# Kernel tuning notes

Measured on AMD Instinct MI355X. Metric: run time of the kernel, lower is better.

## Reference

```python
import jax, jax.numpy as jnp
import numpy as np

DIM = 1024
HID = 4096
E = 8
K = 3


def setup_inputs() -> dict:
    key = jax.random.key(0)
    ks = jax.random.split(key, 5)
    x = jax.random.normal(ks[0], (2, 2048, DIM), dtype=jnp.float32)
    # router: nn.Linear(dim, E) -- initialized to zero in source, but we use small
    # random weights so routing is non-degenerate for the correctness baseline.
    router_w = jax.random.normal(ks[1], (E, DIM), dtype=jnp.float32) * 0.02
    router_b = jax.random.normal(ks[2], (E,), dtype=jnp.float32) * 0.02
    # per-expert SwiGLU params: w12: [E, dim, 2*hid], w3: [E, hid, dim]
    w12 = jax.random.normal(ks[3], (E, DIM, 2 * HID), dtype=jnp.float32) * 0.02
    w3 = jax.random.normal(ks[4], (E, HID, DIM), dtype=jnp.float32) * 0.02
    return {"x": x, "router_w": router_w, "router_b": router_b, "w12": w12, "w3": w3}


def _moe(x, router_w, router_b, w12, w3):
    # router logits [B, S, E]
    logits = jnp.einsum("bsd,ed->bse", x, router_w) + router_b
    scores = jax.nn.sigmoid(logits)
    topk_scores, topk_idx = jax.lax.top_k(scores, K)  # [B,S,K]
    weights = topk_scores / (topk_scores.sum(axis=-1, keepdims=True) + 1e-6)
    # dense per-expert combine weight [B, S, E] (zero if expert not selected)
    onehot = jax.nn.one_hot(topk_idx, E, dtype=x.dtype)  # [B,S,K,E]
    dense_w = jnp.einsum("bske,bsk->bse", onehot, weights)
    out = jnp.zeros_like(x)
    for e in range(E):  # small fixed structural loop over experts
        x12 = x @ w12[e]  # [B,S,2H]
        x1, x2 = jnp.split(x12, 2, axis=-1)
        hidden = jax.nn.silu(x1) * x2
        out = out + (hidden @ w3[e]) * dense_w[..., e:e + 1]
    aux_loss = 0.01 * jnp.mean(logits ** 2)
    return out, aux_loss


def reference(x, router_w, router_b, w12, w3):
    return _moe(x, router_w, router_b, w12, w3)
```

## Files before the change

kernel.cpp:

```cpp
#include <hip/hip_runtime.h>
#include <math.h>

typedef unsigned short u16;
typedef __bf16 bf16x8 __attribute__((ext_vector_type(8)));
typedef float f32x4 __attribute__((ext_vector_type(4)));

#define T_TOK 4096
#define DIM   1024
#define HID   4096
#define NE    8
#define TOPK  3
#define NPAIR 12288

#define PREP_W3_BASE  1024
#define PREP_W12_BASE 3072
#define PREP_BLOCKS   7168

constexpr size_t OFF_CTRL = 0;
constexpr size_t OFF_XB   = 256;
constexpr size_t OFF_W12T = OFF_XB   + (size_t)T_TOK * DIM * 2;
constexpr size_t OFF_W3T  = OFF_W12T + (size_t)NE * 2 * HID * DIM * 2;
constexpr size_t OFF_HID  = OFF_W3T  + (size_t)NE * DIM * HID * 2;
constexpr size_t OFF_Y    = OFF_HID  + (size_t)NPAIR * HID * 2;
constexpr size_t OFF_PTOK = OFF_Y    + (size_t)NPAIR * DIM * 4;
constexpr size_t OFF_TE   = OFF_PTOK + (size_t)NPAIR * 4;
constexpr size_t OFF_TW   = OFF_TE   + (size_t)T_TOK * TOPK * 4;
constexpr size_t OFF_TS   = OFF_TW   + (size_t)T_TOK * TOPK * 4;

__device__ __forceinline__ u16 f2bf(float f) {
    unsigned u = __builtin_bit_cast(unsigned, f);
    u += 0x7fffu + ((u >> 16) & 1u);
    return (u16)(u >> 16);
}

__device__ __forceinline__ void ld_g2l(const u16* g, u16* l) {
    __builtin_amdgcn_global_load_lds((__attribute__((address_space(1))) unsigned*)(g),
                                     (__attribute__((address_space(3))) unsigned*)(l),
                                     16, 0, 0);
}

#define VMCNT(N) asm volatile("s_waitcnt vmcnt(" #N ")" ::: "memory")
#define LGKM0  asm volatile("s_waitcnt lgkmcnt(0)" ::: "memory")
#define SBAR   __builtin_amdgcn_s_barrier()
#define SCHED0 __builtin_amdgcn_sched_barrier(0)
#define PRIO1  __builtin_amdgcn_s_setprio(1)
#define PRIO0  __builtin_amdgcn_s_setprio(0)

#define STAGE_A02(dst) { ld_g2l(srcA[0], (dst) + (0 * 64 + wave * 8) * 64); \
                         ld_g2l(srcA[2], (dst) + (2 * 64 + wave * 8) * 64); }
#define STAGE_B01(dst) { ld_g2l(srcB[0], (dst) + 16384 + (0 * 64 + wave * 8) * 64); \
                         ld_g2l(srcB[1], (dst) + 16384 + (1 * 64 + wave * 8) * 64); }
#define STAGE_B23(dst) { ld_g2l(srcB[2], (dst) + 16384 + (2 * 64 + wave * 8) * 64); \
                         ld_g2l(srcB[3], (dst) + 16384 + (3 * 64 + wave * 8) * 64); }
#define STAGE_A13(dst) { ld_g2l(srcA[1], (dst) + (1 * 64 + wave * 8) * 64); \
                         ld_g2l(srcA[3], (dst) + (3 * 64 + wave * 8) * 64); }
#define ADV()          { _Pragma("unroll") \
                         for (int r_ = 0; r_ < 4; ++r_) { srcA[r_] += 64; srcB[r_] += 64; } }

__device__ __forceinline__ void tc_tile(const float* __restrict__ inp,
                                        u16* __restrict__ outp,
                                        int K, int N, int n0, int k0, int tid,
                                        u16 (*lt)[72]) {
    const int k = tid >> 2;
    const int cbase = (tid & 3) * 4;
    const float* row = inp + (size_t)(k0 + k) * N + n0;
#pragma unroll
    for (int j = 0; j < 16; ++j) {
        const int c = cbase + j * 16;
        float4 f = *(const float4*)(row + c);
        lt[c + 0][k] = f2bf(f.x);
        lt[c + 1][k] = f2bf(f.y);
        lt[c + 2][k] = f2bf(f.z);
        lt[c + 3][k] = f2bf(f.w);
    }
    __syncthreads();
    const int rg = tid >> 2;
    const int kc = (tid & 3) * 16;
#pragma unroll
    for (int g = 0; g < 4; ++g) {
        const int n = g * 64 + rg;
        u16* op = outp + (size_t)(n0 + n) * K + k0 + kc;
        *(uint4*)(op)     = *(const uint4*)(&lt[n][kc]);
        *(uint4*)(op + 8) = *(const uint4*)(&lt[n][kc + 8]);
    }
}

__global__ __launch_bounds__(256) void prep_kernel(const float* __restrict__ x,
                                                   const float* __restrict__ rw,
                                                   const float* __restrict__ rb,
                                                   u16* __restrict__ xb,
                                                   int* __restrict__ tok_expert,
                                                   float* __restrict__ tok_w,
                                                   int* __restrict__ ctrl,
                                                   float* __restrict__ aux,
                                                   const float* __restrict__ w12,
                                                   u16* __restrict__ w12t,
                                                   const float* __restrict__ w3,
                                                   u16* __restrict__ w3t) {
    __shared__ __align__(16) u16 lt[256][72];
    const int bid = blockIdx.x;
    const int tid = threadIdx.x;

    if (bid >= PREP_W12_BASE) {
        const int b = bid - PREP_W12_BASE;
        const int z = b >> 9;
        const int r = b & 511;
        const int kt = r >> 5, nt = r & 31;
        tc_tile(w12 + (size_t)z * DIM * 2 * HID, w12t + (size_t)z * DIM * 2 * HID,
                DIM, 2 * HID, nt * 256, kt * 64, tid, lt);
        return;
    }
    if (bid >= PREP_W3_BASE) {
        const int b = bid - PREP_W3_BASE;
        const int z = b >> 8;
        const int r = b & 255;
        const int kt = r >> 2, nt = r & 3;
        tc_tile(w3 + (size_t)z * HID * DIM, w3t + (size_t)z * HID * DIM,
                HID, DIM, nt * 256, kt * 64, tid, lt);
        return;
    }

    int* hist = (int*)&lt[0][0];
    float* auxsh = (float*)&lt[2][0];
    if (tid < NE) hist[tid] = 0;
    if (tid == NE) auxsh[0] = 0.f;
    __syncthreads();

    const int wave = tid >> 6, lane = tid & 63;
    const int t = bid * 4 + wave;
    const float* xr = x + (size_t)t * DIM;
    u16* xbr = xb + (size_t)t * DIM;

    float p[NE];
#pragma unroll
    for (int e = 0; e < NE; e++) p[e] = 0.f;
#pragma unroll
    for (int q = 0; q < 4; ++q) {
        const int d = q * 256 + lane * 4;
        float4 f = *(const float4*)(xr + d);
        uint2 v;
        v.x = (unsigned)f2bf(f.x) | ((unsigned)f2bf(f.y) << 16);
        v.y = (unsigned)f2bf(f.z) | ((unsigned)f2bf(f.w) << 16);
        *(uint2*)(xbr + d) = v;
#pragma unroll
        for (int e = 0; e < NE; e++) {
            float4 w = *(const float4*)(rw + e * DIM + d);
            p[e] += f.x * w.x + f.y * w.y + f.z * w.z + f.w * w.w;
        }
    }
#pragma unroll
    for (int e = 0; e < NE; e++) {
#pragma unroll
        for (int off = 32; off; off >>= 1) p[e] += __shfl_down(p[e], off, 64);
    }
    if (lane == 0) {
        float s[NE]; float auxs = 0.f;
#pragma unroll
        for (int e = 0; e < NE; e++) {
            float lg = p[e] + rb[e];
            auxs += lg * lg;
            s[e] = 1.f / (1.f + __expf(-lg));
        }
        atomicAdd(auxsh, auxs);
        unsigned mask = 0; float wsum = 0.f;
        int idxs[TOPK]; float vals[TOPK];
        for (int k = 0; k < TOPK; k++) {
            float best = -1.f; int bi = 0;
            for (int e = 0; e < NE; e++)
                if (!((mask >> e) & 1u) && s[e] > best) { best = s[e]; bi = e; }
            mask |= 1u << bi; idxs[k] = bi; vals[k] = best; wsum += best;
        }
        wsum += 1e-6f;
        for (int k = 0; k < TOPK; k++) {
            tok_expert[t * TOPK + k] = idxs[k];
            tok_w[t * TOPK + k] = vals[k] / wsum;
            atomicAdd(&hist[idxs[k]], 1);
        }
    }
    __syncthreads();
    if (tid < NE) { int h = hist[tid]; if (h) atomicAdd(&ctrl[tid], h); }
    if (tid == NE) atomicAdd(aux, auxsh[0] * (0.01f / 32768.0f));
}

__global__ __launch_bounds__(256) void assign_kernel(const int* __restrict__ tok_expert,
                                                     int* __restrict__ ctrl,
                                                     int* __restrict__ pair_token,
                                                     int* __restrict__ tok_slot) {
    __shared__ int soff[NE];
    __shared__ int hist[NE];
    __shared__ int base[NE];
    const int tid = threadIdx.x;
    if (tid < NE) {
        int acc = 0;
        for (int i = 0; i < tid; ++i) acc += ctrl[i];
        soff[tid] = acc;
        hist[tid] = 0;
    }
    __syncthreads();
    const int t = blockIdx.x * blockDim.x + tid;
    int e[TOPK], p[TOPK];
#pragma unroll
    for (int k = 0; k < TOPK; k++) {
        e[k] = tok_expert[t * TOPK + k];
        p[k] = atomicAdd(&hist[e[k]], 1);
    }
    __syncthreads();
    if (tid < NE && hist[tid]) base[tid] = atomicAdd(&ctrl[16 + tid], hist[tid]);
    __syncthreads();
#pragma unroll
    for (int k = 0; k < TOPK; k++) {
        const int slot = soff[e[k]] + base[e[k]] + p[k];
        pair_token[slot] = t;
        tok_slot[t * TOPK + k] = slot;
    }
}

__global__ __launch_bounds__(512, 2) void gemm1_kernel(const u16* __restrict__ xb,
                                                       const u16* __restrict__ w12t,
                                                       const int* __restrict__ pair_token,
                                                       const int* __restrict__ ctrl,
                                                       u16* __restrict__ hidden) {
    const int e = blockIdx.z;
    const int cnt = ctrl[e];
    if ((int)blockIdx.y * 256 >= cnt) return;
    int off = 0;
    for (int i = 0; i < e; ++i) off += ctrl[i];
    const int rowbase = off + blockIdx.y * 256;
    const int rowend = off + cnt;
    const int n0 = blockIdx.x * 128;

    extern __shared__ __align__(16) u16 lds[];

    const int tid = threadIdx.x;
    const int wave = tid >> 6, lane = tid & 63;
    const int srow = tid >> 3;
    const int scol = ((tid & 7) ^ (srow & 7)) * 8;

    const u16* srcA[4];
    const u16* srcB[4];
#pragma unroll
    for (int r = 0; r < 4; ++r) {
        int sr = rowbase + r * 64 + srow;
        int tok = (sr < rowend) ? pair_token[sr] : 0;
        srcA[r] = xb + (size_t)tok * DIM + scol;
    }
#pragma unroll
    for (int r = 0; r < 2; ++r) {
        srcB[r]     = w12t + ((size_t)e * 2 * HID + n0 + r * 64 + srow) * DIM + scol;
        srcB[r + 2] = srcB[r] + (size_t)HID * DIM;
    }

    const int wm = wave >> 2, wn = wave & 3;
    const int lrow = lane & 15, lq = lane >> 4, xm = lrow & 7;
    const int so0 = ((lq ^ xm) << 3);
    const int so1 = (((4 | lq) ^ xm) << 3);

    f32x4 acc0[8][2], acc1[8][2];
#pragma unroll
    for (int mf = 0; mf < 8; ++mf)
#pragma unroll
        for (int nf = 0; nf < 2; ++nf) { acc0[mf][nf] = (f32x4)0.f; acc1[mf][nf] = (f32x4)0.f; }

    STAGE_A02(lds); STAGE_B01(lds);
    STAGE_B23(lds);
    STAGE_A13(lds);
    ADV();

    const int NT = DIM / 64;
    for (int kt = 0; kt < NT; ++kt) {
        u16* cur = lds + (kt & 1) * 32768;
        u16* nxt = lds + ((kt & 1) ^ 1) * 32768;
        const u16* sA = cur;
        const u16* sB = cur + 16384;
        const bool notlast = (kt < NT - 1);

        bf16x8 a[4][2], b0[2][2], b1[2][2];
        VMCNT(4); SBAR; SCHED0;
#pragma unroll
        for (int mf = 0; mf < 4; ++mf) {
            const u16* base = sA + (wm * 128 + mf * 16 + lrow) * 64;
            a[mf][0] = *(const bf16x8*)(base + so0);
            a[mf][1] = *(const bf16x8*)(base + so1);
        }
#pragma unroll
        for (int nf = 0; nf < 2; ++nf) {
            const u16* base = sB + (wn * 32 + nf * 16 + lrow) * 64;
            b0[nf][0] = *(const bf16x8*)(base + so0);
            b0[nf][1] = *(const bf16x8*)(base + so1);
        }
        if (notlast) { STAGE_A02(nxt); STAGE_B01(nxt); }
        LGKM0; SCHED0;
        PRIO1;
#pragma unroll
        for (int mf = 0; mf < 4; ++mf)
#pragma unroll
            for (int nf = 0; nf < 2; ++nf) {
                acc0[mf][nf] = __builtin_amdgcn_mfma_f32_16x16x32_bf16(a[mf][0], b0[nf][0], acc0[mf][nf], 0, 0, 0);
                acc0[mf][nf] = __builtin_amdgcn_mfma_f32_16x16x32_bf16(a[mf][1], b0[nf][1], acc0[mf][nf], 0, 0, 0);
            }
        PRIO0;
        if (notlast) { VMCNT(6); } else { VMCNT(2); }
        SBAR; SCHED0;
#pragma unroll
        for (int nf = 0; nf < 2; ++nf) {
            const u16* base = sB + 128 * 64 + (wn * 32 + nf * 16 + lrow) * 64;
            b1[nf][0] = *(const bf16x8*)(base + so0);
            b1[nf][1] = *(const bf16x8*)(base + so1);
        }
        if (notlast) STAGE_B23(nxt);
        LGKM0; SCHED0;
        PRIO1;
#pragma unroll
        for (int mf = 0; mf < 4; ++mf)
#pragma unroll
            for (int nf = 0; nf < 2; ++nf) {
                acc1[mf][nf] = __builtin_amdgcn_mfma_f32_16x16x32_bf16(a[mf][0], b1[nf][0], acc1[mf][nf], 0, 0, 0);
                acc1[mf][nf] = __builtin_amdgcn_mfma_f32_16x16x32_bf16(a[mf][1], b1[nf][1], acc1[mf][nf], 0, 0, 0);
            }
        PRIO0;
        if (notlast) { VMCNT(6); } else { VMCNT(0); }
        SBAR; SCHED0;
#pragma unroll
        for (int mf = 0; mf < 4; ++mf) {
            const u16* base = sA + (wm * 128 + (mf + 4) * 16 + lrow) * 64;
            a[mf][0] = *(const bf16x8*)(base + so0);
            a[mf][1] = *(const bf16x8*)(base + so1);
        }
        if (notlast) { STAGE_A13(nxt); ADV(); }
        LGKM0; SCHED0;
        PRIO1;
#pragma unroll
        for (int mf = 0; mf < 4; ++mf)
#pragma unroll
            for (int nf = 0; nf < 2; ++nf) {
                acc1[mf + 4][nf] = __builtin_amdgcn_mfma_f32_16x16x32_bf16(a[mf][0], b1[nf][0], acc1[mf + 4][nf], 0, 0, 0);
                acc1[mf + 4][nf] = __builtin_amdgcn_mfma_f32_16x16x32_bf16(a[mf][1], b1[nf][1], acc1[mf + 4][nf], 0, 0, 0);
            }
        PRIO0;
        SBAR;
        PRIO1;
#pragma unroll
        for (int mf = 0; mf < 4; ++mf)
#pragma unroll
            for (int nf = 0; nf < 2; ++nf) {
                acc0[mf + 4][nf] = __builtin_amdgcn_mfma_f32_16x16x32_bf16(a[mf][0], b0[nf][0], acc0[mf + 4][nf], 0, 0, 0);
                acc0[mf + 4][nf] = __builtin_amdgcn_mfma_f32_16x16x32_bf16(a[mf][1], b0[nf][1], acc0[mf + 4][nf], 0, 0, 0);
            }
        PRIO0;
    }

#pragma unroll
    for (int mf = 0; mf < 8; ++mf) {
        const int gr0 = rowbase + wm * 128 + mf * 16 + lq * 4;
#pragma unroll
        for (int nf = 0; nf < 2; ++nf) {
            const int gc = n0 + wn * 32 + nf * 16 + lrow;
#pragma unroll
            for (int r = 0; r < 4; ++r) {
                const int gr = gr0 + r;
                if (gr < rowend) {
                    float x1 = acc0[mf][nf][r], x2 = acc1[mf][nf][r];
                    float h = x1 / (1.f + __expf(-x1)) * x2;
                    hidden[(size_t)gr * HID + gc] = f2bf(h);
                }
            }
        }
    }
}

__global__ __launch_bounds__(512, 2) void gemm2_kernel(const u16* __restrict__ hidden,
                                                       const u16* __restrict__ w3t,
                                                       const int* __restrict__ ctrl,
                                                       float* __restrict__ ybuf) {
    const int e = blockIdx.z;
    const int cnt = ctrl[e];
    if ((int)blockIdx.y * 256 >= cnt) return;
    int off = 0;
    for (int i = 0; i < e; ++i) off += ctrl[i];
    const int rowbase = off + blockIdx.y * 256;
    const int rowend = off + cnt;
    const int n0 = blockIdx.x * 256;

    extern __shared__ __align__(16) u16 lds[];

    const int tid = threadIdx.x;
    const int wave = tid >> 6, lane = tid & 63;
    const int srow = tid >> 3;
    const int scol = ((tid & 7) ^ (srow & 7)) * 8;

    const u16* srcA[4];
    const u16* srcB[4];
#pragma unroll
    for (int r = 0; r < 4; ++r) {
        int sr = rowbase + r * 64 + srow;
        if (sr > NPAIR - 1) sr = NPAIR - 1;
        srcA[r] = hidden + (size_t)sr * HID + scol;
        srcB[r] = w3t + ((size_t)e * DIM + n0 + r * 64 + srow) * HID + scol;
    }

    const int wm = wave >> 2, wn = wave & 3;
    const int lrow = lane & 15, lq = lane >> 4, xm = lrow & 7;
    const int so0 = ((lq ^ xm) << 3);
    const int so1 = (((4 | lq) ^ xm) << 3);

    f32x4 acc[8][4];
#pragma unroll
    for (int mf = 0; mf < 8; ++mf)
#pragma unroll
        for (int nf = 0; nf < 4; ++nf) acc[mf][nf] = (f32x4)0.f;

    STAGE_A02(lds); STAGE_B01(lds);
    STAGE_B23(lds);
    STAGE_A13(lds);
    ADV();

    const int NT = HID / 64;
    for (int kt = 0; kt < NT; ++kt) {
        u16* cur = lds + (kt & 1) * 32768;
        u16* nxt = lds + ((kt & 1) ^ 1) * 32768;
        const u16* sA = cur;
        const u16* sB = cur + 16384;
        const bool notlast = (kt < NT - 1);

        bf16x8 a[4][2], b[4][2];
        VMCNT(4); SBAR; SCHED0;
#pragma unroll
        for (int mf = 0; mf < 4; ++mf) {
            const u16* base = sA + (wm * 128 + mf * 16 + lrow) * 64;
            a[mf][0] = *(const bf16x8*)(base + so0);
            a[mf][1] = *(const bf16x8*)(base + so1);
        }
#pragma unroll
        for (int nf = 0; nf < 2; ++nf) {
            const u16* base = sB + (nf * 64 + wn * 16 + lrow) * 64;
            b[nf][0] = *(const bf16x8*)(base + so0);
            b[nf][1] = *(const bf16x8*)(base + so1);
        }
        if (notlast) { STAGE_A02(nxt); STAGE_B01(nxt); }
        LGKM0; SCHED0;
        PRIO1;
#pragma unroll
        for (int mf = 0; mf < 4; ++mf)
#pragma unroll
            for (int nf = 0; nf < 2; ++nf) {
                acc[mf][nf] = __builtin_amdgcn_mfma_f32_16x16x32_bf16(a[mf][0], b[nf][0], acc[mf][nf], 0, 0, 0);
                acc[mf][nf] = __builtin_amdgcn_mfma_f32_16x16x32_bf16(a[mf][1], b[nf][1], acc[mf][nf], 0, 0, 0);
            }
        PRIO0;
        if (notlast) { VMCNT(6); } else { VMCNT(2); }
        SBAR; SCHED0;
#pragma unroll
        for (int nf = 2; nf < 4; ++nf) {
            const u16* base = sB + (nf * 64 + wn * 16 + lrow) * 64;
            b[nf][0] = *(const bf16x8*)(base + so0);
            b[nf][1] = *(const bf16x8*)(base + so1);
        }
        if (notlast) STAGE_B23(nxt);
        LGKM0; SCHED0;
        PRIO1;
#pragma unroll
        for (int mf = 0; mf < 4; ++mf)
#pragma unroll
            for (int nf = 2; nf < 4; ++nf) {
                acc[mf][nf] = __builtin_amdgcn_mfma_f32_16x16x32_bf16(a[mf][0], b[nf][0], acc[mf][nf], 0, 0, 0);
                acc[mf][nf] = __builtin_amdgcn_mfma_f32_16x16x32_bf16(a[mf][1], b[nf][1], acc[mf][nf], 0, 0, 0);
            }
        PRIO0;
        if (notlast) { VMCNT(6); } else { VMCNT(0); }
        SBAR; SCHED0;
#pragma unroll
        for (int mf = 0; mf < 4; ++mf) {
            const u16* base = sA + (wm * 128 + (mf + 4) * 16 + lrow) * 64;
            a[mf][0] = *(const bf16x8*)(base + so0);
            a[mf][1] = *(const bf16x8*)(base + so1);
        }
        if (notlast) { STAGE_A13(nxt); ADV(); }
        LGKM0; SCHED0;
        PRIO1;
#pragma unroll
        for (int mf = 0; mf < 4; ++mf)
#pragma unroll
            for (int nf = 2; nf < 4; ++nf) {
                acc[mf + 4][nf] = __builtin_amdgcn_mfma_f32_16x16x32_bf16(a[mf][0], b[nf][0], acc[mf + 4][nf], 0, 0, 0);
                acc[mf + 4][nf] = __builtin_amdgcn_mfma_f32_16x16x32_bf16(a[mf][1], b[nf][1], acc[mf + 4][nf], 0, 0, 0);
            }
        PRIO0;
        SBAR;
        PRIO1;
#pragma unroll
        for (int mf = 0; mf < 4; ++mf)
#pragma unroll
            for (int nf = 0; nf < 2; ++nf) {
                acc[mf + 4][nf] = __builtin_amdgcn_mfma_f32_16x16x32_bf16(a[mf][0], b[nf][0], acc[mf + 4][nf], 0, 0, 0);
                acc[mf + 4][nf] = __builtin_amdgcn_mfma_f32_16x16x32_bf16(a[mf][1], b[nf][1], acc[mf + 4][nf], 0, 0, 0);
            }
        PRIO0;
    }

#pragma unroll
    for (int mf = 0; mf < 8; ++mf) {
        const int gr0 = rowbase + wm * 128 + mf * 16 + lq * 4;
#pragma unroll
        for (int nf = 0; nf < 4; ++nf) {
            const int gc = n0 + nf * 64 + wn * 16 + lrow;
#pragma unroll
            for (int r = 0; r < 4; ++r) {
                const int gr = gr0 + r;
                if (gr < rowend) ybuf[(size_t)gr * DIM + gc] = acc[mf][nf][r];
            }
        }
    }
}

__global__ __launch_bounds__(256) void combine_kernel(const float* __restrict__ ybuf,
                                                      const int* __restrict__ tok_slot,
                                                      const float* __restrict__ tok_w,
                                                      float* __restrict__ out) {
    const int t = blockIdx.x;
    const int d = threadIdx.x * 4;
    const int s0 = tok_slot[t * 3 + 0], s1 = tok_slot[t * 3 + 1], s2 = tok_slot[t * 3 + 2];
    const float w0 = tok_w[t * 3 + 0], w1 = tok_w[t * 3 + 1], w2 = tok_w[t * 3 + 2];
    const float4 a0 = *(const float4*)(ybuf + (size_t)s0 * DIM + d);
    const float4 a1 = *(const float4*)(ybuf + (size_t)s1 * DIM + d);
    const float4 a2 = *(const float4*)(ybuf + (size_t)s2 * DIM + d);
    float4 o;
    o.x = w0 * a0.x + w1 * a1.x + w2 * a2.x;
    o.y = w0 * a0.y + w1 * a1.y + w2 * a2.y;
    o.z = w0 * a0.z + w1 * a1.z + w2 * a2.z;
    o.w = w0 * a0.w + w1 * a1.w + w2 * a2.w;
    *(float4*)(out + (size_t)t * DIM + d) = o;
}

extern "C" void kernel_launch(void* const* d_in, const int* in_sizes, int n_in,
                              void* d_out, int out_size, void* d_ws, size_t ws_size,
                              hipStream_t stream) {
    const float* x   = (const float*)d_in[0];
    const float* rw  = (const float*)d_in[1];
    const float* rb  = (const float*)d_in[2];
    const float* w12 = (const float*)d_in[3];
    const float* w3  = (const float*)d_in[4];
    float* out = (float*)d_out;
    char* ws = (char*)d_ws;

    int*   ctrl       = (int*)(ws + OFF_CTRL);
    u16*   xb         = (u16*)(ws + OFF_XB);
    u16*   w12t       = (u16*)(ws + OFF_W12T);
    u16*   w3t        = (u16*)(ws + OFF_W3T);
    u16*   hidden     = (u16*)(ws + OFF_HID);
    float* ybuf       = (float*)(ws + OFF_Y);
    int*   pair_token = (int*)(ws + OFF_PTOK);
    int*   tok_expert = (int*)(ws + OFF_TE);
    float* tok_w      = (float*)(ws + OFF_TW);
    int*   tok_slot   = (int*)(ws + OFF_TS);

    static bool attr_set = false;
    if (!attr_set) {
        hipFuncSetAttribute((const void*)gemm1_kernel, hipFuncAttributeMaxDynamicSharedMemorySize, 131072);
        hipFuncSetAttribute((const void*)gemm2_kernel, hipFuncAttributeMaxDynamicSharedMemorySize, 131072);
        attr_set = true;
    }

    hipMemsetAsync(ctrl, 0, 256, stream);
    hipMemsetAsync(out + (size_t)T_TOK * DIM, 0, sizeof(float), stream);

    prep_kernel<<<PREP_BLOCKS, 256, 0, stream>>>(x, rw, rb, xb, tok_expert, tok_w, ctrl,
                                                 out + (size_t)T_TOK * DIM, w12, w12t, w3, w3t);
    assign_kernel<<<16, 256, 0, stream>>>(tok_expert, ctrl, pair_token, tok_slot);

    gemm1_kernel<<<dim3(HID / 128, 16, NE), 512, 131072, stream>>>(xb, w12t, pair_token, ctrl, hidden);
    gemm2_kernel<<<dim3(DIM / 256, 16, NE), 512, 131072, stream>>>(hidden, w3t, ctrl, ybuf);
    combine_kernel<<<T_TOK, 256, 0, stream>>>(ybuf, tok_slot, tok_w, out);
    (void)in_sizes; (void)n_in; (void)out_size; (void)ws_size;
}
```

Measured before the change: 805.4 us.

## Move w3 weight transpose into gemm1 launch and persist w12 transpose blocks

The w3 fp32-to-bf16 transpose leaves the prep kernel and runs as an extra z-slice of the gemm1 grid, so it overlaps with the expert GEMM1 work. The w12 transpose now uses 256 blocks that each loop over 16 k-tiles, replacing 4096 one-shot blocks and cutting the prep grid. This removes serialized weight-conversion time before gemm1 and reduces block launch overhead. The risk is that the transpose blocks compete with GEMM blocks for CUs and LDS, and the fewer w12 blocks may leave the prep phase with less parallelism.

```diff
diff --git a/kernel.cpp b/kernel.cpp
--- a/kernel.cpp
+++ b/kernel.cpp
@@ -12,9 +12,8 @@
 #define TOPK  3
 #define NPAIR 12288
 
-#define PREP_W3_BASE  1024
-#define PREP_W12_BASE 3072
-#define PREP_BLOCKS   7168
+#define PREP_RTR_BASE 256
+#define PREP_BLOCKS   1280
 
 constexpr size_t OFF_CTRL = 0;
 constexpr size_t OFF_XB   = 256;
@@ -57,10 +56,10 @@
 #define ADV()          { _Pragma("unroll") \
                          for (int r_ = 0; r_ < 4; ++r_) { srcA[r_] += 64; srcB[r_] += 64; } }
 
-__device__ __forceinline__ void tc_tile(const float* __restrict__ inp,
-                                        u16* __restrict__ outp,
-                                        int K, int N, int n0, int k0, int tid,
-                                        u16 (*lt)[72]) {
+__device__ __forceinline__ void tc_tile256(const float* __restrict__ inp,
+                                           u16* __restrict__ outp,
+                                           int K, int N, int n0, int k0, int tid,
+                                           u16 (*lt)[72]) {
     const int k = tid >> 2;
     const int cbase = (tid & 3) * 4;
     const float* row = inp + (size_t)(k0 + k) * N + n0;
@@ -94,29 +93,20 @@
                                                    int* __restrict__ ctrl,
                                                    float* __restrict__ aux,
                                                    const float* __restrict__ w12,
-                                                   u16* __restrict__ w12t,
-                                                   const float* __restrict__ w3,
-                                                   u16* __restrict__ w3t) {
+                                                   u16* __restrict__ w12t) {
     __shared__ __align__(16) u16 lt[256][72];
     const int bid = blockIdx.x;
     const int tid = threadIdx.x;
 
-    if (bid >= PREP_W12_BASE) {
-        const int b = bid - PREP_W12_BASE;
-        const int z = b >> 9;
-        const int r = b & 511;
-        const int kt = r >> 5, nt = r & 31;
-        tc_tile(w12 + (size_t)z * DIM * 2 * HID, w12t + (size_t)z * DIM * 2 * HID,
-                DIM, 2 * HID, nt * 256, kt * 64, tid, lt);
-        return;
-    }
-    if (bid >= PREP_W3_BASE) {
-        const int b = bid - PREP_W3_BASE;
-        const int z = b >> 8;
-        const int r = b & 255;
-        const int kt = r >> 2, nt = r & 3;
-        tc_tile(w3 + (size_t)z * HID * DIM, w3t + (size_t)z * HID * DIM,
-                HID, DIM, nt * 256, kt * 64, tid, lt);
+    if (bid < PREP_RTR_BASE) {
+        const int z = bid >> 5;
+        const int nt = bid & 31;
+        const float* src = w12 + (size_t)z * DIM * 2 * HID;
+        u16* dst = w12t + (size_t)z * DIM * 2 * HID;
+        for (int kt = 0; kt < 16; ++kt) {
+            tc_tile256(src, dst, DIM, 2 * HID, nt * 256, kt * 64, tid, lt);
+            __syncthreads();
+        }
         return;
     }
 
@@ -127,7 +117,7 @@
     __syncthreads();
 
     const int wave = tid >> 6, lane = tid & 63;
-    const int t = bid * 4 + wave;
+    const int t = (bid - PREP_RTR_BASE) * 4 + wave;
     const float* xr = x + (size_t)t * DIM;
     u16* xbr = xb + (size_t)t * DIM;
 
@@ -219,7 +209,49 @@
                                                        const u16* __restrict__ w12t,
                                                        const int* __restrict__ pair_token,
                                                        const int* __restrict__ ctrl,
-                                                       u16* __restrict__ hidden) {
+                                                       u16* __restrict__ hidden,
+                                                       const float* __restrict__ w3,
+                                                       u16* __restrict__ w3t) {
+    extern __shared__ __align__(16) u16 lds[];
+    const int tid = threadIdx.x;
+
+    if (blockIdx.z == 8) {
+        u16 (*lt)[72] = (u16(*)[72])lds;
+        const int t9 = blockIdx.y * 32 + blockIdx.x;
+        const int e9 = t9 >> 6;
+        const int r9 = t9 & 63;
+        const int nt = r9 >> 4;
+        const int ktg = r9 & 15;
+        const float* src = w3 + (size_t)e9 * HID * DIM;
+        u16* dst = w3t + (size_t)e9 * HID * DIM;
+        const int n0 = nt * 256;
+        for (int i = 0; i < 4; ++i) {
+            const int k0 = (ktg * 4 + i) * 64;
+            const int kr = tid >> 3;
+            const int cb = (tid & 7) * 4;
+            const float* row = src + (size_t)(k0 + kr) * DIM + n0;
+#pragma unroll
+            for (int j = 0; j < 8; ++j) {
+                const int c = cb + j * 32;
+                float4 f = *(const float4*)(row + c);
+                lt[c + 0][kr] = f2bf(f.x);
+                lt[c + 1][kr] = f2bf(f.y);
+                lt[c + 2][kr] = f2bf(f.z);
+                lt[c + 3][kr] = f2bf(f.w);
+            }
+            __syncthreads();
+            const int n = tid >> 1;
+            const int kc = (tid & 1) * 32;
+            u16* op = dst + (size_t)(n0 + n) * HID + k0 + kc;
+            *(uint4*)(op)      = *(const uint4*)(&lt[n][kc]);
+            *(uint4*)(op + 8)  = *(const uint4*)(&lt[n][kc + 8]);
+            *(uint4*)(op + 16) = *(const uint4*)(&lt[n][kc + 16]);
+            *(uint4*)(op + 24) = *(const uint4*)(&lt[n][kc + 24]);
+            __syncthreads();
+        }
+        return;
+    }
+
     const int e = blockIdx.z;
     const int cnt = ctrl[e];
     if ((int)blockIdx.y * 256 >= cnt) return;
@@ -229,9 +261,6 @@
     const int rowend = off + cnt;
     const int n0 = blockIdx.x * 128;
 
-    extern __shared__ __align__(16) u16 lds[];
-
-    const int tid = threadIdx.x;
     const int wave = tid >> 6, lane = tid & 63;
     const int srow = tid >> 3;
     const int scol = ((tid & 7) ^ (srow & 7)) * 8;
@@ -564,10 +593,11 @@
     hipMemsetAsync(out + (size_t)T_TOK * DIM, 0, sizeof(float), stream);
 
     prep_kernel<<<PREP_BLOCKS, 256, 0, stream>>>(x, rw, rb, xb, tok_expert, tok_w, ctrl,
-                                                 out + (size_t)T_TOK * DIM, w12, w12t, w3, w3t);
+                                                 out + (size_t)T_TOK * DIM, w12, w12t);
     assign_kernel<<<16, 256, 0, stream>>>(tok_expert, ctrl, pair_token, tok_slot);
 
-    gemm1_kernel<<<dim3(HID / 128, 16, NE), 512, 131072, stream>>>(xb, w12t, pair_token, ctrl, hidden);
+    gemm1_kernel<<<dim3(HID / 128, 16, 9), 512, 131072, stream>>>(xb, w12t, pair_token, ctrl,
+                                                                  hidden, w3, w3t);
     gemm2_kernel<<<dim3(DIM / 256, 16, NE), 512, 131072, stream>>>(hidden, w3t, ctrl, ybuf);
     combine_kernel<<<T_TOK, 256, 0, stream>>>(ybuf, tok_slot, tok_w, out);
     (void)in_sizes; (void)n_in; (void)out_size; (void)ws_size;
```

New measurement: 792.9 us. No clear change (-1.5%).
